# Kernel tuning notes

Measured on AMD Instinct MI355X. Metric: run time of the kernel, lower is better.

## Reference

```python
import jax, jax.numpy as jnp
import numpy as np

ALPHA, KL, KS = 0.2, 0.3, 1.0  # PGDKernel defaults

_OFFSETS = jnp.array([[a, b, c] for a in (0, 1) for b in (0, 1) for c in (0, 1)], dtype=jnp.int32)  # [8,3]


def _cic_corners(pos, mesh):
    # pos: [N,3] in grid units, periodic wrap
    base = jnp.floor(pos)
    frac = pos - base                              # [N,3]
    base = base.astype(jnp.int32)
    idx = (base[:, None, :] + _OFFSETS[None, :, :]) % mesh   # [N,8,3]
    w = jnp.prod(jnp.where(_OFFSETS[None].astype(bool), frac[:, None, :], 1.0 - frac[:, None, :]), axis=-1)  # [N,8]
    flat = (idx[..., 0] * mesh + idx[..., 1]) * mesh + idx[..., 2]  # [N,8]
    return flat, w


def cic_paint(pos, mesh):
    flat, w = _cic_corners(pos, mesh)
    grid = jnp.zeros((mesh * mesh * mesh,), dtype=pos.dtype)
    grid = grid.at[flat.reshape(-1)].add(w.reshape(-1))
    return grid.reshape(mesh, mesh, mesh)


def cic_read(grid, pos, mesh):
    flat, w = _cic_corners(pos, mesh)
    return jnp.sum(grid.reshape(-1)[flat] * w, axis=-1)  # [N]


def fftk(mesh):
    k = (2.0 * np.pi * jnp.fft.fftfreq(mesh)).astype(jnp.float32)
    return [k.reshape(-1, 1, 1), k.reshape(1, -1, 1), k.reshape(1, 1, -1)]


def setup_inputs() -> dict:
    key = jax.random.key(0)
    k1, k2 = jax.random.split(key)
    mesh = 128
    n = mesh ** 3
    g = jnp.arange(mesh, dtype=jnp.float32)
    lattice = jnp.stack(jnp.meshgrid(g, g, g, indexing='ij'), axis=-1).reshape(-1, 3)
    pos = (lattice + 0.5 * jax.random.normal(k1, (n, 3), dtype=jnp.float32)) % mesh
    vel = 0.01 * jax.random.normal(k2, (n, 3), dtype=jnp.float32)
    return {"pos": pos, "vel": vel, "mesh_size": mesh}


def reference(pos, vel, mesh_size):
    mesh = int(mesh_size)
    delta = cic_paint(pos, mesh)                       # particle-mesh deposit
    delta_k = jnp.fft.fftn(delta)                      # complex64 [m,m,m]
    kvec = fftk(mesh)
    kk = sum(ki ** 2 for ki in kvec)
    kk_safe = jnp.where(kk == 0, 1.0, kk)
    pgd_range = jnp.exp(-(KL ** 2) / kk_safe) * jnp.exp(-(kk ** 2) / (KS ** 4))
    pgd_range = jnp.where(kk == 0, 0.0, pgd_range)
    invlap = -jnp.where(kk == 0, 0.0, 1.0 / kk_safe)   # inverse laplace kernel
    pot_k = delta_k * (invlap * pgd_range)
    # gradient kernel: i*k_i ; force_i = readout(ifft(-grad_i * pot_k))
    forces = jnp.stack(
        [cic_read(jnp.fft.ifftn(-1j * ki * pot_k).real.astype(pos.dtype), pos, mesh) for ki in kvec],
        axis=-1,
    )  # [N,3]
    new_pos = pos + ALPHA * forces
    return new_pos, vel
```

## Files before the change

### kernel.cpp

```cpp
#include <hip/hip_runtime.h>
#include <hip/hip_bf16.h>

#define MESH   128
#define MESH2  16384
#define MESH3  2097152
#define SXT 13
#define SYT 9
#define SZT 38
#define CELLS (SXT * SYT * SZT)

__device__ __forceinline__ float kfreq(int i) {
    int s = (i < 64) ? i : (i - 128);
    return 0.049087385212340517f * (float)s;
}

__device__ __forceinline__ float load_elem(const void* p, int i, int isbf16) {
    if (isbf16) return __bfloat162float(((const __hip_bfloat16*)p)[i]);
    return ((const float*)p)[i];
}

__device__ __forceinline__ void dft8(float2* a, float sgn) {
    const float r = 0.70710678118654752f;
    float2 b0 = a[0], b1 = a[4], b2 = a[2], b3 = a[6];
    float2 b4 = a[1], b5 = a[5], b6 = a[3], b7 = a[7];
    float2 c0 = make_float2(b0.x + b1.x, b0.y + b1.y);
    float2 c1 = make_float2(b0.x - b1.x, b0.y - b1.y);
    float2 c2 = make_float2(b2.x + b3.x, b2.y + b3.y);
    float2 c3 = make_float2(b2.x - b3.x, b2.y - b3.y);
    float2 c4 = make_float2(b4.x + b5.x, b4.y + b5.y);
    float2 c5 = make_float2(b4.x - b5.x, b4.y - b5.y);
    float2 c6 = make_float2(b6.x + b7.x, b6.y + b7.y);
    float2 c7 = make_float2(b6.x - b7.x, b6.y - b7.y);
    float2 t3 = make_float2(-sgn * c3.y, sgn * c3.x);
    float2 t7 = make_float2(-sgn * c7.y, sgn * c7.x);
    float2 d0 = make_float2(c0.x + c2.x, c0.y + c2.y);
    float2 d2 = make_float2(c0.x - c2.x, c0.y - c2.y);
    float2 d1 = make_float2(c1.x + t3.x, c1.y + t3.y);
    float2 d3 = make_float2(c1.x - t3.x, c1.y - t3.y);
    float2 d4 = make_float2(c4.x + c6.x, c4.y + c6.y);
    float2 d6 = make_float2(c4.x - c6.x, c4.y - c6.y);
    float2 d5 = make_float2(c5.x + t7.x, c5.y + t7.y);
    float2 d7 = make_float2(c5.x - t7.x, c5.y - t7.y);
    float2 w1 = make_float2(r, sgn * r), w3 = make_float2(-r, sgn * r);
    float2 t5 = make_float2(d5.x * w1.x - d5.y * w1.y, d5.x * w1.y + d5.y * w1.x);
    float2 t6 = make_float2(-sgn * d6.y, sgn * d6.x);
    float2 t7b = make_float2(d7.x * w3.x - d7.y * w3.y, d7.x * w3.y + d7.y * w3.x);
    a[0] = make_float2(d0.x + d4.x, d0.y + d4.y);
    a[4] = make_float2(d0.x - d4.x, d0.y - d4.y);
    a[1] = make_float2(d1.x + t5.x, d1.y + t5.y);
    a[5] = make_float2(d1.x - t5.x, d1.y - t5.y);
    a[2] = make_float2(d2.x + t6.x, d2.y + t6.y);
    a[6] = make_float2(d2.x - t6.x, d2.y - t6.y);
    a[3] = make_float2(d3.x + t7b.x, d3.y + t7b.y);
    a[7] = make_float2(d3.x - t7b.x, d3.y - t7b.y);
}

__global__ void detect_kernel(const unsigned int* __restrict__ words,
                              int* __restrict__ flag) {
    int t = threadIdx.x;
    unsigned long long m = __ballot((words[t] >> 15) & 1u);
    if (t == 0) *flag = (__popcll(m) > 16) ? 0 : 1;
}

__global__ __launch_bounds__(256)
void paint_lds(const void* __restrict__ pos, float* __restrict__ grid,
               const int* __restrict__ flag) {
    __shared__ float tile[CELLS];
    int t = threadIdx.x;
    int bi = blockIdx.x;
    int tz = bi & 3, ty = (bi >> 2) & 31, tx = bi >> 7;
    int x0 = tx * 8, y0 = ty * 4, z0 = tz * 32;
    for (int i = t; i < CELLS; i += 256) tile[i] = 0.f;
    __syncthreads();
    int isbf16 = *flag;
#pragma unroll
    for (int it = 0; it < 4; ++it) {
        int pi = t + 256 * it;
        int dz = pi & 31, dy = (pi >> 5) & 3, dx = pi >> 7;
        int p = (((x0 + dx) << 7) + (y0 + dy)) * 128 + z0 + dz;
        float P0 = load_elem(pos, 3 * p + 0, isbf16);
        float P1 = load_elem(pos, 3 * p + 1, isbf16);
        float P2 = load_elem(pos, 3 * p + 2, isbf16);
        float f0 = floorf(P0), f1 = floorf(P1), f2 = floorf(P2);
        int ix = (int)f0, iy = (int)f1, iz = (int)f2;
        float wx1 = P0 - f0, wy1 = P1 - f1, wz1 = P2 - f2;
        float wx0 = 1.f - wx1, wy0 = 1.f - wy1, wz0 = 1.f - wz1;
        int lx = (ix - x0 + 2) & 127, ly = (iy - y0 + 2) & 127;
        int lz = (iz - z0 + 2) & 127;
        if (lx <= 11 && ly <= 7 && lz <= 36) {
            int b00 = (lx * SYT + ly) * SZT + lz;
            int b01 = b00 + SZT;
            int b10 = b00 + SYT * SZT;
            int b11 = b10 + SZT;
            atomicAdd(&tile[b00],     wx0 * wy0 * wz0);
            atomicAdd(&tile[b00 + 1], wx0 * wy0 * wz1);
            atomicAdd(&tile[b01],     wx0 * wy1 * wz0);
            atomicAdd(&tile[b01 + 1], wx0 * wy1 * wz1);
            atomicAdd(&tile[b10],     wx1 * wy0 * wz0);
            atomicAdd(&tile[b10 + 1], wx1 * wy0 * wz1);
            atomicAdd(&tile[b11],     wx1 * wy1 * wz0);
            atomicAdd(&tile[b11 + 1], wx1 * wy1 * wz1);
        } else {
            int gx = ix & 127, gy = iy & 127, gz = iz & 127;
            int hx = (gx + 1) & 127, hy = (gy + 1) & 127, hz = (gz + 1) & 127;
            atomicAdd(&grid[((gx << 7) + gy) * 128 + gz], wx0 * wy0 * wz0);
            atomicAdd(&grid[((gx << 7) + gy) * 128 + hz], wx0 * wy0 * wz1);
            atomicAdd(&grid[((gx << 7) + hy) * 128 + gz], wx0 * wy1 * wz0);
            atomicAdd(&grid[((gx << 7) + hy) * 128 + hz], wx0 * wy1 * wz1);
            atomicAdd(&grid[((hx << 7) + gy) * 128 + gz], wx1 * wy0 * wz0);
            atomicAdd(&grid[((hx << 7) + gy) * 128 + hz], wx1 * wy0 * wz1);
            atomicAdd(&grid[((hx << 7) + hy) * 128 + gz], wx1 * wy1 * wz0);
            atomicAdd(&grid[((hx << 7) + hy) * 128 + hz], wx1 * wy1 * wz1);
        }
    }
    __syncthreads();
    for (int i = t; i < CELLS; i += 256) {
        float v = tile[i];
        if (v != 0.f) {
            int lx = i / (SYT * SZT);
            int r  = i - lx * (SYT * SZT);
            int ly = r / SZT, lz = r - ly * SZT;
            int gx = (x0 - 2 + lx) & 127, gy = (y0 - 2 + ly) & 127;
            int gz = (z0 - 2 + lz) & 127;
            atomicAdd(&grid[((gx << 7) + gy) * 128 + gz], v);
        }
    }
}

template<int AXIS, int INV, int LM, int SM>
__global__ __launch_bounds__(256)
void fft8x16(const void* __restrict__ srcv, void* __restrict__ dstv) {
    __shared__ float2 Z[16 * 137];
    int t = threadIdx.x;
    int l = (AXIS == 2) ? (t >> 4) : (t & 15);
    int u = (AXIS == 2) ? (t & 15) : (t >> 4);
    int L = blockIdx.x * 16 + l;
    const float sgn = INV ? 1.f : -1.f;
    const float invN3 = 1.0f / 2097152.0f;
    long base; int es;
    if (AXIS == 2)      { base = (long)L * 128; es = 1; }
    else if (AXIS == 1) { base = (long)(L >> 7) * 16384 + (L & 127); es = 128; }
    else                { base = (long)L; es = 16384; }

    float2 v[8];
#pragma unroll
    for (int n1 = 0; n1 < 8; ++n1) {
        int e = 16 * n1 + u;
        float2 x;
        if (LM == 1) x = make_float2(((const float*)srcv)[base + (long)e * es], 0.f);
        else         x = ((const float2*)srcv)[base + (long)e * es];
        if (LM == 2) { float k = kfreq(e) * invN3; x = make_float2(k * x.y, -k * x.x); }
        v[n1] = x;
    }
    dft8(v, sgn);
#pragma unroll
    for (int k1 = 0; k1 < 8; ++k1) {
        float ang = sgn * 0.049087385212340517f * (float)(u * k1);
        float sn, cs; __sincosf(ang, &sn, &cs);
        float2 y = v[k1];
        Z[l * 137 + k1 * 17 + u] =
            make_float2(y.x * cs - y.y * sn, y.x * sn + y.y * cs);
    }
    __syncthreads();

    int k1 = u & 7, c = u >> 3;
    float2 w[8];
#pragma unroll
    for (int b = 0; b < 8; ++b) {
        float2 za = Z[l * 137 + k1 * 17 + b];
        float2 zb = Z[l * 137 + k1 * 17 + 8 + b];
        float2 s = c ? make_float2(za.x - zb.x, za.y - zb.y)
                     : make_float2(za.x + zb.x, za.y + zb.y);
        if (c && b) {
            float ang = sgn * 0.39269908169872414f * (float)b;
            float sn, cs; __sincosf(ang, &sn, &cs);
            s = make_float2(s.x * cs - s.y * sn, s.x * sn + s.y * cs);
        }
        w[b] = s;
    }
    dft8(w, sgn);
#pragma unroll
    for (int k3 = 0; k3 < 8; ++k3) {
        int k = u + 16 * k3;
        float2 vv = w[k3];
        if (SM == 1) {
            float kx = kfreq(k), ky = kfreq(L >> 7), kz = kfreq(L & 127);
            float kk = kx * kx + ky * ky + kz * kz;
            float f = 0.f;
            if (kk > 0.f) f = -__expf(-0.09f / kk - kk * kk) / kk;
            vv.x *= f; vv.y *= f;
        }
        if (SM == 2) ((float*)dstv)[base + (long)k * es] = vv.x;
        else         ((float2*)dstv)[base + (long)k * es] = vv;
    }
}

__global__ __launch_bounds__(256)
void update_kernel(const void* __restrict__ pos, const void* __restrict__ vel,
                   const float* __restrict__ Fx, const float* __restrict__ Fy,
                   const float* __restrict__ Fz, float* __restrict__ out,
                   const int* __restrict__ flag, int n) {
    int p = blockIdx.x * blockDim.x + threadIdx.x;
    if (p >= n) return;
    int isbf16 = *flag;
    float P0 = load_elem(pos, 3 * p + 0, isbf16);
    float P1 = load_elem(pos, 3 * p + 1, isbf16);
    float P2 = load_elem(pos, 3 * p + 2, isbf16);
    float f0 = floorf(P0), f1 = floorf(P1), f2 = floorf(P2);
    int ix = ((int)f0) & 127, iy = ((int)f1) & 127, iz = ((int)f2) & 127;
    float wx1 = P0 - f0, wy1 = P1 - f1, wz1 = P2 - f2;
    float wx0 = 1.f - wx1, wy0 = 1.f - wy1, wz0 = 1.f - wz1;
    int jx = (ix + 1) & 127, jy = (iy + 1) & 127, jz = (iz + 1) & 127;
    int b00 = (ix * MESH + iy) * MESH;
    int b01 = (ix * MESH + jy) * MESH;
    int b10 = (jx * MESH + iy) * MESH;
    int b11 = (jx * MESH + jy) * MESH;
    float fx = 0.f, fy = 0.f, fz = 0.f;
    int f; float w;
    f = b00 + iz; w = wx0 * wy0 * wz0; fx += w * Fx[f]; fy += w * Fy[f]; fz += w * Fz[f];
    f = b00 + jz; w = wx0 * wy0 * wz1; fx += w * Fx[f]; fy += w * Fy[f]; fz += w * Fz[f];
    f = b01 + iz; w = wx0 * wy1 * wz0; fx += w * Fx[f]; fy += w * Fy[f]; fz += w * Fz[f];
    f = b01 + jz; w = wx0 * wy1 * wz1; fx += w * Fx[f]; fy += w * Fy[f]; fz += w * Fz[f];
    f = b10 + iz; w = wx1 * wy0 * wz0; fx += w * Fx[f]; fy += w * Fy[f]; fz += w * Fz[f];
    f = b10 + jz; w = wx1 * wy0 * wz1; fx += w * Fx[f]; fy += w * Fy[f]; fz += w * Fz[f];
    f = b11 + iz; w = wx1 * wy1 * wz0; fx += w * Fx[f]; fy += w * Fy[f]; fz += w * Fz[f];
    f = b11 + jz; w = wx1 * wy1 * wz1; fx += w * Fx[f]; fy += w * Fy[f]; fz += w * Fz[f];
    out[3 * p + 0] = P0 + 0.2f * fx;
    out[3 * p + 1] = P1 + 0.2f * fy;
    out[3 * p + 2] = P2 + 0.2f * fz;
    int N3 = 3 * n;
    out[N3 + 3 * p + 0] = load_elem(vel, 3 * p + 0, isbf16);
    out[N3 + 3 * p + 1] = load_elem(vel, 3 * p + 1, isbf16);
    out[N3 + 3 * p + 2] = load_elem(vel, 3 * p + 2, isbf16);
}

extern "C" void kernel_launch(void* const* d_in, const int* in_sizes, int n_in,
                              void* d_out, int out_size, void* d_ws, size_t ws_size,
                              hipStream_t stream) {
    int n = in_sizes[0] / 3;
    const void* pos = d_in[0];
    const void* vel = d_in[1];
    float* out = (float*)d_out;

    char* ws = (char*)d_ws;
    int*    flag = (int*)ws;
    float2* A  = (float2*)(ws + 4096);
    float*  F0 = (float*)(ws + 4096 + 16777216);
    float*  F1 = (float*)(ws + 4096 + 25165824);
    float*  F2 = (float*)(ws + 4096);
    float*  delta = F0;
    float2* S0 = (float2*)d_out;
    float2* S1 = (float2*)((char*)d_out + 16777216);

    detect_kernel<<<1, 64, 0, stream>>>((const unsigned int*)pos, flag);
    hipMemsetAsync(delta, 0, MESH3 * sizeof(float), stream);
    paint_lds<<<2048, 256, 0, stream>>>(pos, delta, flag);

    fft8x16<2, 0, 1, 0><<<1024, 256, 0, stream>>>(delta, A);
    fft8x16<1, 0, 0, 0><<<1024, 256, 0, stream>>>(A, A);
    fft8x16<0, 0, 0, 1><<<1024, 256, 0, stream>>>(A, A);

    fft8x16<2, 1, 0, 0><<<1024, 256, 0, stream>>>(A, S0);
    fft8x16<1, 1, 0, 0><<<1024, 256, 0, stream>>>(S0, S1);
    fft8x16<0, 1, 2, 2><<<1024, 256, 0, stream>>>(S1, F0);
    fft8x16<0, 1, 0, 0><<<1024, 256, 0, stream>>>(S0, S1);
    fft8x16<1, 1, 2, 2><<<1024, 256, 0, stream>>>(S1, F1);
    fft8x16<1, 1, 0, 0><<<1024, 256, 0, stream>>>(A, S0);
    fft8x16<0, 1, 0, 0><<<1024, 256, 0, stream>>>(S0, S1);
    fft8x16<2, 1, 2, 2><<<1024, 256, 0, stream>>>(S1, F2);

    update_kernel<<<(n + 255) / 256, 256, 0, stream>>>(pos, vel, F0, F1, F2, out, flag, n);
}
```

Measured before the change: 308.4 us.

## Pack force components into two complex IFFTs and enlarge paint tiles

```diff
diff --git a/kernel.cpp b/kernel.cpp
--- a/kernel.cpp
+++ b/kernel.cpp
@@ -4,10 +4,8 @@
 #define MESH   128
 #define MESH2  16384
 #define MESH3  2097152
-#define SXT 13
-#define SYT 9
-#define SZT 38
-#define CELLS (SXT * SYT * SZT)
+#define SP 21
+#define CELLS (SP * SP * SP)
 
 __device__ __forceinline__ float kfreq(int i) {
     int s = (i < 64) ? i : (i - 128);
@@ -68,15 +66,15 @@
     __shared__ float tile[CELLS];
     int t = threadIdx.x;
     int bi = blockIdx.x;
-    int tz = bi & 3, ty = (bi >> 2) & 31, tx = bi >> 7;
-    int x0 = tx * 8, y0 = ty * 4, z0 = tz * 32;
+    int tz = bi & 7, ty = (bi >> 3) & 7, tx = bi >> 6;
+    int x0 = tx * 16, y0 = ty * 16, z0 = tz * 16;
     for (int i = t; i < CELLS; i += 256) tile[i] = 0.f;
     __syncthreads();
     int isbf16 = *flag;
 #pragma unroll
-    for (int it = 0; it < 4; ++it) {
+    for (int it = 0; it < 16; ++it) {
         int pi = t + 256 * it;
-        int dz = pi & 31, dy = (pi >> 5) & 3, dx = pi >> 7;
+        int dz = pi & 15, dy = (pi >> 4) & 15, dx = pi >> 8;
         int p = (((x0 + dx) << 7) + (y0 + dy)) * 128 + z0 + dz;
         float P0 = load_elem(pos, 3 * p + 0, isbf16);
         float P1 = load_elem(pos, 3 * p + 1, isbf16);
@@ -87,11 +85,11 @@
         float wx0 = 1.f - wx1, wy0 = 1.f - wy1, wz0 = 1.f - wz1;
         int lx = (ix - x0 + 2) & 127, ly = (iy - y0 + 2) & 127;
         int lz = (iz - z0 + 2) & 127;
-        if (lx <= 11 && ly <= 7 && lz <= 36) {
-            int b00 = (lx * SYT + ly) * SZT + lz;
-            int b01 = b00 + SZT;
-            int b10 = b00 + SYT * SZT;
-            int b11 = b10 + SZT;
+        if (lx <= 19 && ly <= 19 && lz <= 19) {
+            int b00 = (lx * SP + ly) * SP + lz;
+            int b01 = b00 + SP;
+            int b10 = b00 + SP * SP;
+            int b11 = b10 + SP;
             atomicAdd(&tile[b00],     wx0 * wy0 * wz0);
             atomicAdd(&tile[b00 + 1], wx0 * wy0 * wz1);
             atomicAdd(&tile[b01],     wx0 * wy1 * wz0);
@@ -117,9 +115,9 @@
     for (int i = t; i < CELLS; i += 256) {
         float v = tile[i];
         if (v != 0.f) {
-            int lx = i / (SYT * SZT);
-            int r  = i - lx * (SYT * SZT);
-            int ly = r / SZT, lz = r - ly * SZT;
+            int lx = i / (SP * SP);
+            int r  = i - lx * (SP * SP);
+            int ly = r / SP, lz = r - ly * SP;
             int gx = (x0 - 2 + lx) & 127, gy = (y0 - 2 + ly) & 127;
             int gz = (z0 - 2 + lz) & 127;
             atomicAdd(&grid[((gx << 7) + gy) * 128 + gz], v);
@@ -129,28 +127,28 @@
 
 template<int AXIS, int INV, int LM, int SM>
 __global__ __launch_bounds__(256)
-void fft8x16(const void* __restrict__ srcv, void* __restrict__ dstv) {
+void fft8x16(const void* __restrict__ s0, const void* __restrict__ s1,
+             void* __restrict__ d0, void* __restrict__ d1, void* __restrict__ d2) {
     __shared__ float2 Z[16 * 137];
     int t = threadIdx.x;
     int l = (AXIS == 2) ? (t >> 4) : (t & 15);
     int u = (AXIS == 2) ? (t & 15) : (t >> 4);
     int L = blockIdx.x * 16 + l;
+    int vol = blockIdx.y;
     const float sgn = INV ? 1.f : -1.f;
     const float invN3 = 1.0f / 2097152.0f;
     long base; int es;
     if (AXIS == 2)      { base = (long)L * 128; es = 1; }
     else if (AXIS == 1) { base = (long)(L >> 7) * 16384 + (L & 127); es = 128; }
     else                { base = (long)L; es = 16384; }
+    const void* srcv = vol ? s1 : s0;
 
     float2 v[8];
 #pragma unroll
     for (int n1 = 0; n1 < 8; ++n1) {
         int e = 16 * n1 + u;
-        float2 x;
-        if (LM == 1) x = make_float2(((const float*)srcv)[base + (long)e * es], 0.f);
-        else         x = ((const float2*)srcv)[base + (long)e * es];
-        if (LM == 2) { float k = kfreq(e) * invN3; x = make_float2(k * x.y, -k * x.x); }
-        v[n1] = x;
+        if (LM == 1) v[n1] = make_float2(((const float*)srcv)[base + (long)e * es], 0.f);
+        else         v[n1] = ((const float2*)srcv)[base + (long)e * es];
     }
     dft8(v, sgn);
 #pragma unroll
@@ -183,23 +181,33 @@
     for (int k3 = 0; k3 < 8; ++k3) {
         int k = u + 16 * k3;
         float2 vv = w[k3];
-        if (SM == 1) {
+        long idx = base + (long)k * es;
+        if (SM == 0) {
+            ((float2*)(vol ? d1 : d0))[idx] = vv;
+        } else if (SM == 3) {
             float kx = kfreq(k), ky = kfreq(L >> 7), kz = kfreq(L & 127);
             float kk = kx * kx + ky * ky + kz * kz;
             float f = 0.f;
-            if (kk > 0.f) f = -__expf(-0.09f / kk - kk * kk) / kk;
-            vv.x *= f; vv.y *= f;
-        }
-        if (SM == 2) ((float*)dstv)[base + (long)k * es] = vv.x;
-        else         ((float2*)dstv)[base + (long)k * es] = vv;
-    }
-}
-
-__global__ __launch_bounds__(256)
-void update_kernel(const void* __restrict__ pos, const void* __restrict__ vel,
-                   const float* __restrict__ Fx, const float* __restrict__ Fy,
-                   const float* __restrict__ Fz, float* __restrict__ out,
-                   const int* __restrict__ flag, int n) {
+            if (kk > 0.f) f = -__expf(-0.09f / kk - kk * kk) / kk * invN3;
+            float a = vv.x * f, b = vv.y * f;
+            ((float2*)d0)[idx] = make_float2(-kx * b - ky * a, kx * a - ky * b);
+            ((float2*)d1)[idx] = make_float2(-kz * b, kz * a);
+        } else {
+            if (vol == 0) {
+                ((float*)d0)[idx] = vv.x;
+                ((float*)d1)[idx] = vv.y;
+            } else {
+                ((float*)d2)[idx] = vv.x;
+            }
+        }
+    }
+}
+
+__global__ __launch_bounds__(256)
+void update_pos(const void* __restrict__ pos,
+                const float* __restrict__ Fx, const float* __restrict__ Fy,
+                const float* __restrict__ Fz, float* __restrict__ out,
+                const int* __restrict__ flag, int n) {
     int p = blockIdx.x * blockDim.x + threadIdx.x;
     if (p >= n) return;
     int isbf16 = *flag;
@@ -228,10 +236,18 @@
     out[3 * p + 0] = P0 + 0.2f * fx;
     out[3 * p + 1] = P1 + 0.2f * fy;
     out[3 * p + 2] = P2 + 0.2f * fz;
-    int N3 = 3 * n;
-    out[N3 + 3 * p + 0] = load_elem(vel, 3 * p + 0, isbf16);
-    out[N3 + 3 * p + 1] = load_elem(vel, 3 * p + 1, isbf16);
-    out[N3 + 3 * p + 2] = load_elem(vel, 3 * p + 2, isbf16);
+}
+
+__global__ __launch_bounds__(256)
+void copy_vel(const void* __restrict__ vel, float* __restrict__ dst,
+              const int* __restrict__ flag, int m) {
+    int i0 = (blockIdx.x * blockDim.x + threadIdx.x) * 4;
+    int isbf16 = *flag;
+#pragma unroll
+    for (int j = 0; j < 4; ++j) {
+        int i = i0 + j;
+        if (i < m) dst[i] = load_elem(vel, i, isbf16);
+    }
 }
 
 extern "C" void kernel_launch(void* const* d_in, const int* in_sizes, int n_in,
@@ -245,29 +261,25 @@
     char* ws = (char*)d_ws;
     int*    flag = (int*)ws;
     float2* A  = (float2*)(ws + 4096);
-    float*  F0 = (float*)(ws + 4096 + 16777216);
-    float*  F1 = (float*)(ws + 4096 + 25165824);
-    float*  F2 = (float*)(ws + 4096);
-    float*  delta = F0;
-    float2* S0 = (float2*)d_out;
-    float2* S1 = (float2*)((char*)d_out + 16777216);
+    float*  F0 = (float*)(ws + 4096 + (16u << 20));
+    float*  F1 = (float*)(ws + 4096 + (24u << 20));
+    float*  delta = (float*)d_out;
+    float2* G2 = (float2*)((char*)d_out + (24u << 20));
+    float*  F2 = (float*)((char*)d_out + (40u << 20));
 
     detect_kernel<<<1, 64, 0, stream>>>((const unsigned int*)pos, flag);
     hipMemsetAsync(delta, 0, MESH3 * sizeof(float), stream);
-    paint_lds<<<2048, 256, 0, stream>>>(pos, delta, flag);
-
-    fft8x16<2, 0, 1, 0><<<1024, 256, 0, stream>>>(delta, A);
-    fft8x16<1, 0, 0, 0><<<1024, 256, 0, stream>>>(A, A);
-    fft8x16<0, 0, 0, 1><<<1024, 256, 0, stream>>>(A, A);
-
-    fft8x16<2, 1, 0, 0><<<1024, 256, 0, stream>>>(A, S0);
-    fft8x16<1, 1, 0, 0><<<1024, 256, 0, stream>>>(S0, S1);
-    fft8x16<0, 1, 2, 2><<<1024, 256, 0, stream>>>(S1, F0);
-    fft8x16<0, 1, 0, 0><<<1024, 256, 0, stream>>>(S0, S1);
-    fft8x16<1, 1, 2, 2><<<1024, 256, 0, stream>>>(S1, F1);
-    fft8x16<1, 1, 0, 0><<<1024, 256, 0, stream>>>(A, S0);
-    fft8x16<0, 1, 0, 0><<<1024, 256, 0, stream>>>(S0, S1);
-    fft8x16<2, 1, 2, 2><<<1024, 256, 0, stream>>>(S1, F2);
-
-    update_kernel<<<(n + 255) / 256, 256, 0, stream>>>(pos, vel, F0, F1, F2, out, flag, n);
-}
+    paint_lds<<<512, 256, 0, stream>>>(pos, delta, flag);
+
+    fft8x16<2, 0, 1, 0><<<dim3(1024, 1), 256, 0, stream>>>(delta, nullptr, A, nullptr, nullptr);
+    fft8x16<1, 0, 0, 0><<<dim3(1024, 1), 256, 0, stream>>>(A, nullptr, A, nullptr, nullptr);
+    fft8x16<0, 0, 0, 3><<<dim3(1024, 1), 256, 0, stream>>>(A, nullptr, A, G2, nullptr);
+
+    fft8x16<2, 1, 0, 0><<<dim3(1024, 2), 256, 0, stream>>>(A, G2, A, G2, nullptr);
+    fft8x16<1, 1, 0, 0><<<dim3(1024, 2), 256, 0, stream>>>(A, G2, A, G2, nullptr);
+    fft8x16<0, 1, 0, 4><<<dim3(1024, 2), 256, 0, stream>>>(A, G2, F0, F1, F2);
+
+    update_pos<<<(n + 255) / 256, 256, 0, stream>>>(pos, F0, F1, F2, out, flag, n);
+    int m = 3 * n;
+    copy_vel<<<(m / 4 + 255) / 256, 256, 0, stream>>>(vel, out + m, flag, m);
+}
```

New measurement: 300.5 us. 2.6% less time.
